# Performance work log

Hardware: AMD Instinct MI355X
Metric: run time of the kernel (lower is better)

The kernel has to match this reference:

```python
import jax, jax.numpy as jnp
from jax import lax
import numpy as np

NPOINTS = 1024
B, N, C = 32, 100000, 3


def setup_inputs() -> dict:
    key = jax.random.key(0)
    k1, k2 = jax.random.split(key)
    coord = jax.random.normal(k1, (B, N, C), dtype=jnp.float32)
    farthest_init = jax.random.randint(k2, (B,), 0, N, dtype=jnp.int64)
    return {"coord": coord, "farthest_init": farthest_init}


def reference(coord, farthest_init):
    # coord: (B, N, 3); farthest_init: (B,) seed indices.
    Bs, Ns, _ = coord.shape
    init_distance = jnp.full((Bs, Ns), 1e10, dtype=coord.dtype)

    def step(carry, _):
        distance, farthest = carry
        # gather current centroid per batch: (B, 1, 3)
        centroid = jnp.take_along_axis(coord, farthest[:, None, None], axis=1)
        dist = jnp.sum((coord - centroid) ** 2, axis=-1)  # (B, N)
        distance = jnp.minimum(distance, dist)            # masked update
        new_farthest = jnp.argmax(distance, axis=-1)      # (B,)
        # record the index that was just used as centroid (pre-update), as in torch loop
        return (distance, new_farthest), farthest

    (_, _), centroids_t = lax.scan(step, (init_distance, farthest_init), None, length=NPOINTS)
    centroids = centroids_t.T  # (B, NPOINTS)
    # gather sampled coordinates: (B, NPOINTS, 3)
    sampled = jnp.take_along_axis(coord, centroids[:, :, None], axis=1)
    return centroids, sampled
```

## Files before the change

### kernel.cpp

```cpp
#include <hip/hip_runtime.h>
#include <stdint.h>

#define BATCHES 32
#define NPT     100000
#define NSAMP   1024
#define GPB     16
#define NPAIR   16
#define TPB     1024
#define NCW     15
#define CTH     (NCW*64)
#define PPB     6250
#define PPT     7
#define TAILT   490

typedef unsigned long long u64;
typedef unsigned int u32;

#define WS_BYTES (2 * BATCHES * GPB * 4 * 8)

__device__ __forceinline__ void red_ki(u64& key, u32& idx, int off) {
    u64 ok = __shfl_xor(key, off, 64);
    u32 oi = __shfl_xor(idx, off, 64);
    if (ok > key || (ok == key && oi < idx)) { key = ok; idx = oi; }
}

__device__ __forceinline__ void red_step(u64& key, u32& idx, float& x, float& y, float& z, int off) {
    u64   ok = __shfl_xor(key, off, 64);
    u32   oi = __shfl_xor(idx, off, 64);
    float ox = __shfl_xor(x, off, 64);
    float oy = __shfl_xor(y, off, 64);
    float oz = __shfl_xor(z, off, 64);
    if (ok > key || (ok == key && oi < idx)) { key = ok; idx = oi; x = ox; y = oy; z = oz; }
}

__global__ void
__attribute__((amdgpu_flat_work_group_size(TPB, TPB), amdgpu_waves_per_eu(4, 4)))
fps_kernel(const float* __restrict__ coord,
           const int* __restrict__ seed_raw,
           float* __restrict__ out,
           u64* __restrict__ rec)
{
    const int tid  = threadIdx.x;
    const int lane = tid & 63;
    const int wid  = tid >> 6;
    const int p    = (int)blockIdx.x & (NPAIR - 1);
    const int g    = (int)blockIdx.x >> 4;
    const int base = g * PPB;
    const int bA = p, bB = p + NPAIR;

    __shared__ u64 winw[2][2][2];
    __shared__ u32 sbar[8];
    __shared__ u64   pkey[2][NCW];
    __shared__ u32   pidx[2][NCW];
    __shared__ float pxs[2][NCW], pys[2][NCW], pzs[2][NCW];

    if (tid < 8) { sbar[tid] = 0; ((u64*)winw)[tid] = 0ull; }
    __syncthreads();

    float* cent_out = out;
    float* samp_out = out + BATCHES * NSAMP;

    if (wid == NCW) {
        for (int t = 1; t < NSAMP; ++t) {
            #pragma unroll
            for (int xb = 0; xb < 2; ++xb) {
                const int batch = xb ? bB : bA;
                u64* slot = rec + ((size_t)((t & 1) * BATCHES + batch) * GPB) * 4;
                const u64 t2 = (u64)(((t >> 1) + 1) & 3);
                const bool mine = lane < 3 * GPB;
                u64* wp = slot + (mine ? ((lane / 3) * 4 + (lane % 3)) : 0);
                u64 w = 0;
                for (;;) {
                    bool ok = true;
                    if (mine) {
                        w = __hip_atomic_load(wp, __ATOMIC_RELAXED, __HIP_MEMORY_SCOPE_AGENT);
                        ok = (w >> 62) == t2;
                    }
                    if (__ballot(ok) == ~0ull) break;
                    __builtin_amdgcn_s_sleep(1);
                }
                const int li = lane & 15;
                u64 w0 = __shfl(w, 3 * li + 0, 64);
                u64 w1 = __shfl(w, 3 * li + 1, 64);
                u64 w2 = __shfl(w, 3 * li + 2, 64);
                u64 k3 = 0ull; u32 i3 = 0xFFFFFFFFu; float x3 = 0.f, y3 = 0.f, z3 = 0.f;
                if (lane < GPB) {
                    k3 = (w0 & 0x3FFFFFFFFFFFFFFFull) | (((w1 >> 60) & 3ull) << 62);
                    u32 xbt = (u32)(w1 >> 28);
                    u32 ybt = (u32)(((w1 & 0xFFFFFFFull) << 4) | ((w2 >> 58) & 0xFull));
                    u32 zbt = (u32)(w2 >> 26);
                    i3 = (u32)((w2 >> 9) & 0x1FFFFu);
                    x3 = __uint_as_float(xbt); y3 = __uint_as_float(ybt); z3 = __uint_as_float(zbt);
                }
                red_step(k3, i3, x3, y3, z3, 8); red_step(k3, i3, x3, y3, z3, 4);
                red_step(k3, i3, x3, y3, z3, 2); red_step(k3, i3, x3, y3, z3, 1);
                if (lane == 0) {
                    u32 xbt = __float_as_uint(x3), ybt = __float_as_uint(y3), zbt = __float_as_uint(z3);
                    u64 v0 = (t2 << 62) | ((u64)xbt << 30) | (u64)(ybt >> 2);
                    u64 v1 = (t2 << 62) | ((u64)(ybt & 3u) << 60) | ((u64)zbt << 28) | ((u64)i3 << 11);
                    __hip_atomic_store(&winw[xb][t & 1][0], v0, __ATOMIC_RELAXED, __HIP_MEMORY_SCOPE_WORKGROUP);
                    __hip_atomic_store(&winw[xb][t & 1][1], v1, __ATOMIC_RELAXED, __HIP_MEMORY_SCOPE_WORKGROUP);
                }
            }
        }
        return;
    }

    const int ct = tid;
    const float* cbA = coord + (size_t)bA * (NPT * 3);
    const float* cbB = coord + (size_t)bB * (NPT * 3);

    int odd = 0;
    #pragma unroll
    for (int i = 1; i < 32; i += 2) odd |= seed_raw[i];
    u32 scur[2]; float scx[2], scy[2], scz[2];
    scur[0] = (u32)((odd == 0) ? seed_raw[2 * bA] : seed_raw[bA]);
    scur[1] = (u32)((odd == 0) ? seed_raw[2 * bB] : seed_raw[bB]);
    scx[0] = cbA[(size_t)scur[0] * 3 + 0]; scy[0] = cbA[(size_t)scur[0] * 3 + 1]; scz[0] = cbA[(size_t)scur[0] * 3 + 2];
    scx[1] = cbB[(size_t)scur[1] * 3 + 0]; scy[1] = cbB[(size_t)scur[1] * 3 + 1]; scz[1] = cbB[(size_t)scur[1] * 3 + 2];

    float  px[2][PPT], py[2][PPT], pz[2][PPT];
    double d[2][PPT];
    #pragma unroll
    for (int xb = 0; xb < 2; ++xb) {
        const float* cb = xb ? cbB : cbA;
        #pragma unroll
        for (int k = 0; k < PPT; ++k) {
            bool v = (k < PPT - 1) || (ct < TAILT);
            int gi = base + (v ? (k * CTH + ct) : 0);
            px[xb][k] = v ? cb[(size_t)gi * 3 + 0] : 0.f;
            py[xb][k] = v ? cb[(size_t)gi * 3 + 1] : 0.f;
            pz[xb][k] = v ? cb[(size_t)gi * 3 + 2] : 0.f;
            d[xb][k]  = v ? 1.0e10 : 0.0;
        }
    }

    for (int t = 0; t < NSAMP; ++t) {
        #pragma unroll
        for (int xb = 0; xb < 2; ++xb) {
            const int batch = xb ? bB : bA;
            const int pi = 2 * t + xb;
            u32 cur; float cx, cy, cz;
            if (t == 0) {
                cur = scur[xb]; cx = scx[xb]; cy = scy[xb]; cz = scz[xb];
            } else {
                const u64 t2 = (u64)(((t >> 1) + 1) & 3);
                u64 v0, v1;
                for (;;) {
                    v0 = __hip_atomic_load(&winw[xb][t & 1][0], __ATOMIC_RELAXED, __HIP_MEMORY_SCOPE_WORKGROUP);
                    v1 = __hip_atomic_load(&winw[xb][t & 1][1], __ATOMIC_RELAXED, __HIP_MEMORY_SCOPE_WORKGROUP);
                    if (((v0 >> 62) == t2) & ((v1 >> 62) == t2)) break;
                }
                u32 xbt = (u32)(v0 >> 30);
                u32 ybt = (u32)(((v0 & 0x3FFFFFFFull) << 2) | ((v1 >> 60) & 3ull));
                u32 zbt = (u32)(v1 >> 28);
                cur = (u32)((v1 >> 11) & 0x1FFFFu);
                cx = __uint_as_float(xbt); cy = __uint_as_float(ybt); cz = __uint_as_float(zbt);
            }
            if (g == 0 && wid == 1 && lane == 0) {
                cent_out[batch * NSAMP + t] = (float)cur;
                size_t so = ((size_t)batch * NSAMP + t) * 3;
                samp_out[so + 0] = cx; samp_out[so + 1] = cy; samp_out[so + 2] = cz;
            }
            if (t == NSAMP - 1) continue;

            const double cxd = (double)cx, cyd = (double)cy, czd = (double)cz;
            double bd = -1.0; u32 bi = 0; float bx = 0.f, by = 0.f, bz = 0.f;
            #pragma unroll
            for (int k = 0; k < PPT; ++k) {
                if (k == PPT - 1 && ct >= TAILT) break;
                double dx = __dsub_rn((double)px[xb][k], cxd);
                double dy = __dsub_rn((double)py[xb][k], cyd);
                double dz = __dsub_rn((double)pz[xb][k], czd);
                double d2 = __dadd_rn(__dadd_rn(__dmul_rn(dx, dx), __dmul_rn(dy, dy)),
                                      __dmul_rn(dz, dz));
                double nd = fmin(d[xb][k], d2);
                d[xb][k] = nd;
                bool gt = nd > bd;
                bd = gt ? nd : bd;
                bi = gt ? (u32)(base + k * CTH + ct) : bi;
                bx = gt ? px[xb][k] : bx;
                by = gt ? py[xb][k] : by;
                bz = gt ? pz[xb][k] : bz;
            }
            u64 key = (u64)__double_as_longlong(bd);

            u64 wk = key; u32 wi = bi;
            red_ki(wk, wi, 32); red_ki(wk, wi, 16); red_ki(wk, wi, 8);
            red_ki(wk, wi, 4);  red_ki(wk, wi, 2);  red_ki(wk, wi, 1);
            const int pb = pi & 1;
            if (wi == bi) { pkey[pb][wid] = wk; pidx[pb][wid] = wi;
                            pxs[pb][wid] = bx; pys[pb][wid] = by; pzs[pb][wid] = bz; }

            if (lane == 0)
                __hip_atomic_fetch_add(&sbar[pi & 7], 1u, __ATOMIC_RELEASE, __HIP_MEMORY_SCOPE_WORKGROUP);
            const u32 tgt = (u32)(NCW * ((pi >> 3) + 1));
            while (__hip_atomic_load(&sbar[pi & 7], __ATOMIC_ACQUIRE, __HIP_MEMORY_SCOPE_WORKGROUP) < tgt) {}

            if (wid == 0) {
                u64   k2 = (lane < NCW) ? pkey[pb][lane] : 0ull;
                u32   i2 = (lane < NCW) ? pidx[pb][lane] : 0xFFFFFFFFu;
                float x2 = (lane < NCW) ? pxs[pb][lane] : 0.f;
                float y2 = (lane < NCW) ? pys[pb][lane] : 0.f;
                float z2 = (lane < NCW) ? pzs[pb][lane] : 0.f;
                red_step(k2, i2, x2, y2, z2, 8); red_step(k2, i2, x2, y2, z2, 4);
                red_step(k2, i2, x2, y2, z2, 2); red_step(k2, i2, x2, y2, z2, 1);
                if (lane == 0) {
                    const u32 v = (u32)(t + 1);
                    const u64 t2p = (u64)(((v >> 1) + 1) & 3);
                    u64* r = rec + ((size_t)((v & 1) * BATCHES + batch) * GPB + g) * 4;
                    u32 xbt = __float_as_uint(x2), ybt = __float_as_uint(y2), zbt = __float_as_uint(z2);
                    u64 w0 = (t2p << 62) | (k2 & 0x3FFFFFFFFFFFFFFFull);
                    u64 w1 = (t2p << 62) | ((k2 >> 62) << 60) | ((u64)xbt << 28) | (u64)(ybt >> 4);
                    u64 w2 = (t2p << 62) | ((u64)(ybt & 0xFu) << 58) | ((u64)zbt << 26) | ((u64)i2 << 9);
                    __hip_atomic_store(&r[0], w0, __ATOMIC_RELAXED, __HIP_MEMORY_SCOPE_AGENT);
                    __hip_atomic_store(&r[1], w1, __ATOMIC_RELAXED, __HIP_MEMORY_SCOPE_AGENT);
                    __hip_atomic_store(&r[2], w2, __ATOMIC_RELAXED, __HIP_MEMORY_SCOPE_AGENT);
                }
            }
        }
    }
}

extern "C" void kernel_launch(void* const* d_in, const int* in_sizes, int n_in,
                              void* d_out, int out_size, void* d_ws, size_t ws_size,
                              hipStream_t stream)
{
    const float* coord = (const float*)d_in[0];
    const int*   seed  = (const int*)d_in[1];
    float* out = (float*)d_out;
    u64* rec = (u64*)d_ws;

    hipMemsetAsync(d_ws, 0, WS_BYTES, stream);
    fps_kernel<<<dim3(NPAIR * GPB), dim3(TPB), 0, stream>>>(coord, seed, out, rec);
}
```

Before: 4.390 ms.

## Poll both batches' records together, defer coordinate selection, and narrow barrier wait

The coordinator wave now polls both paired batches' global records in one combined loop, with each lane loading two words. It reduces each batch as soon as that batch's records are ready, instead of waiting on them one after the other. The compute loop no longer carries best-point coordinates through every iteration; only the winning lane recovers them afterwards with a select. The intra-block spin wait is moved so that only wave 0 waits on the counter, letting the other compute waves go ahead to the next step. This cuts polling latency and per-iteration register work, but other waves now rely on the double-buffered shared slots and the later handoff for ordering.

Measured after the change: 7.751 ms. 1.77x slower.

```diff
diff --git a/kernel.cpp b/kernel.cpp
--- a/kernel.cpp
+++ b/kernel.cpp
@@ -62,45 +62,52 @@
 
     if (wid == NCW) {
         for (int t = 1; t < NSAMP; ++t) {
-            #pragma unroll
-            for (int xb = 0; xb < 2; ++xb) {
-                const int batch = xb ? bB : bA;
-                u64* slot = rec + ((size_t)((t & 1) * BATCHES + batch) * GPB) * 4;
-                const u64 t2 = (u64)(((t >> 1) + 1) & 3);
-                const bool mine = lane < 3 * GPB;
-                u64* wp = slot + (mine ? ((lane / 3) * 4 + (lane % 3)) : 0);
-                u64 w = 0;
-                for (;;) {
-                    bool ok = true;
-                    if (mine) {
-                        w = __hip_atomic_load(wp, __ATOMIC_RELAXED, __HIP_MEMORY_SCOPE_AGENT);
-                        ok = (w >> 62) == t2;
+            const u64 t2 = (u64)(((t >> 1) + 1) & 3);
+            const size_t regA = ((size_t)((t & 1) * BATCHES + bA) * GPB) * 4;
+            const size_t regB = ((size_t)((t & 1) * BATCHES + bB) * GPB) * 4;
+            u64* ad = rec + ((lane < 32) ? (regA + 2 * lane) : (regB + 2 * (lane - 32)));
+            bool dA = false, dB = false;
+            u64 wlo = 0, whi = 0;
+            for (;;) {
+                wlo = __hip_atomic_load(&ad[0], __ATOMIC_RELAXED, __HIP_MEMORY_SCOPE_AGENT);
+                whi = __hip_atomic_load(&ad[1], __ATOMIC_RELAXED, __HIP_MEMORY_SCOPE_AGENT);
+                bool ok0 = (wlo >> 62) == t2;
+                bool ok1 = (whi >> 62) == t2;
+                bool ok  = ((lane & 1) == 0) ? (ok0 && ok1) : ok0;
+                u64 bal = __ballot(ok);
+                #pragma unroll
+                for (int xb = 0; xb < 2; ++xb) {
+                    bool done = xb ? dB : dA;
+                    u64 msk = xb ? 0xFFFFFFFF00000000ull : 0x00000000FFFFFFFFull;
+                    if (!done && (bal & msk) == msk) {
+                        const int srcBase = xb ? 32 : 0;
+                        int sj = srcBase + 2 * (lane & 15);
+                        u64 w0 = __shfl(wlo, sj, 64);
+                        u64 w1 = __shfl(whi, sj, 64);
+                        u64 w2 = __shfl(wlo, sj + 1, 64);
+                        u64 k3 = 0ull; u32 i3 = 0xFFFFFFFFu; float x3 = 0.f, y3 = 0.f, z3 = 0.f;
+                        if (lane < GPB) {
+                            k3 = (w0 & 0x3FFFFFFFFFFFFFFFull) | (((w1 >> 60) & 3ull) << 62);
+                            u32 xbt = (u32)(w1 >> 28);
+                            u32 ybt = (u32)(((w1 & 0xFFFFFFFull) << 4) | ((w2 >> 58) & 0xFull));
+                            u32 zbt = (u32)(w2 >> 26);
+                            i3 = (u32)((w2 >> 9) & 0x1FFFFu);
+                            x3 = __uint_as_float(xbt); y3 = __uint_as_float(ybt); z3 = __uint_as_float(zbt);
+                        }
+                        red_step(k3, i3, x3, y3, z3, 8); red_step(k3, i3, x3, y3, z3, 4);
+                        red_step(k3, i3, x3, y3, z3, 2); red_step(k3, i3, x3, y3, z3, 1);
+                        if (lane == 0) {
+                            u32 xbt = __float_as_uint(x3), ybt = __float_as_uint(y3), zbt = __float_as_uint(z3);
+                            u64 v0 = (t2 << 62) | ((u64)xbt << 30) | (u64)(ybt >> 2);
+                            u64 v1 = (t2 << 62) | ((u64)(ybt & 3u) << 60) | ((u64)zbt << 28) | ((u64)i3 << 11);
+                            __hip_atomic_store(&winw[xb][t & 1][0], v0, __ATOMIC_RELAXED, __HIP_MEMORY_SCOPE_WORKGROUP);
+                            __hip_atomic_store(&winw[xb][t & 1][1], v1, __ATOMIC_RELAXED, __HIP_MEMORY_SCOPE_WORKGROUP);
+                        }
+                        if (xb) dB = true; else dA = true;
                     }
-                    if (__ballot(ok) == ~0ull) break;
-                    __builtin_amdgcn_s_sleep(1);
-                }
-                const int li = lane & 15;
-                u64 w0 = __shfl(w, 3 * li + 0, 64);
-                u64 w1 = __shfl(w, 3 * li + 1, 64);
-                u64 w2 = __shfl(w, 3 * li + 2, 64);
-                u64 k3 = 0ull; u32 i3 = 0xFFFFFFFFu; float x3 = 0.f, y3 = 0.f, z3 = 0.f;
-                if (lane < GPB) {
-                    k3 = (w0 & 0x3FFFFFFFFFFFFFFFull) | (((w1 >> 60) & 3ull) << 62);
-                    u32 xbt = (u32)(w1 >> 28);
-                    u32 ybt = (u32)(((w1 & 0xFFFFFFFull) << 4) | ((w2 >> 58) & 0xFull));
-                    u32 zbt = (u32)(w2 >> 26);
-                    i3 = (u32)((w2 >> 9) & 0x1FFFFu);
-                    x3 = __uint_as_float(xbt); y3 = __uint_as_float(ybt); z3 = __uint_as_float(zbt);
-                }
-                red_step(k3, i3, x3, y3, z3, 8); red_step(k3, i3, x3, y3, z3, 4);
-                red_step(k3, i3, x3, y3, z3, 2); red_step(k3, i3, x3, y3, z3, 1);
-                if (lane == 0) {
-                    u32 xbt = __float_as_uint(x3), ybt = __float_as_uint(y3), zbt = __float_as_uint(z3);
-                    u64 v0 = (t2 << 62) | ((u64)xbt << 30) | (u64)(ybt >> 2);
-                    u64 v1 = (t2 << 62) | ((u64)(ybt & 3u) << 60) | ((u64)zbt << 28) | ((u64)i3 << 11);
-                    __hip_atomic_store(&winw[xb][t & 1][0], v0, __ATOMIC_RELAXED, __HIP_MEMORY_SCOPE_WORKGROUP);
-                    __hip_atomic_store(&winw[xb][t & 1][1], v1, __ATOMIC_RELAXED, __HIP_MEMORY_SCOPE_WORKGROUP);
-                }
+                }
+                if (dA && dB) break;
+                __builtin_amdgcn_s_sleep(1);
             }
         }
         return;
@@ -165,7 +172,7 @@
             if (t == NSAMP - 1) continue;
 
             const double cxd = (double)cx, cyd = (double)cy, czd = (double)cz;
-            double bd = -1.0; u32 bi = 0; float bx = 0.f, by = 0.f, bz = 0.f;
+            double bd = -1.0; u32 bi = 0;
             #pragma unroll
             for (int k = 0; k < PPT; ++k) {
                 if (k == PPT - 1 && ct >= TAILT) break;
@@ -179,9 +186,6 @@
                 bool gt = nd > bd;
                 bd = gt ? nd : bd;
                 bi = gt ? (u32)(base + k * CTH + ct) : bi;
-                bx = gt ? px[xb][k] : bx;
-                by = gt ? py[xb][k] : by;
-                bz = gt ? pz[xb][k] : bz;
             }
             u64 key = (u64)__double_as_longlong(bd);
 
@@ -189,15 +193,25 @@
             red_ki(wk, wi, 32); red_ki(wk, wi, 16); red_ki(wk, wi, 8);
             red_ki(wk, wi, 4);  red_ki(wk, wi, 2);  red_ki(wk, wi, 1);
             const int pb = pi & 1;
-            if (wi == bi) { pkey[pb][wid] = wk; pidx[pb][wid] = wi;
-                            pxs[pb][wid] = bx; pys[pb][wid] = by; pzs[pb][wid] = bz; }
+            if (wi == bi) {
+                float bx = px[xb][0], by = py[xb][0], bz = pz[xb][0];
+                #pragma unroll
+                for (int k = 1; k < PPT; ++k) {
+                    bool m = (bi == (u32)(base + k * CTH + ct));
+                    bx = m ? px[xb][k] : bx;
+                    by = m ? py[xb][k] : by;
+                    bz = m ? pz[xb][k] : bz;
+                }
+                pkey[pb][wid] = wk; pidx[pb][wid] = wi;
+                pxs[pb][wid] = bx; pys[pb][wid] = by; pzs[pb][wid] = bz;
+            }
 
             if (lane == 0)
                 __hip_atomic_fetch_add(&sbar[pi & 7], 1u, __ATOMIC_RELEASE, __HIP_MEMORY_SCOPE_WORKGROUP);
-            const u32 tgt = (u32)(NCW * ((pi >> 3) + 1));
-            while (__hip_atomic_load(&sbar[pi & 7], __ATOMIC_ACQUIRE, __HIP_MEMORY_SCOPE_WORKGROUP) < tgt) {}
 
             if (wid == 0) {
+                const u32 tgt = (u32)(NCW * ((pi >> 3) + 1));
+                while (__hip_atomic_load(&sbar[pi & 7], __ATOMIC_ACQUIRE, __HIP_MEMORY_SCOPE_WORKGROUP) < tgt) {}
                 u64   k2 = (lane < NCW) ? pkey[pb][lane] : 0ull;
                 u32   i2 = (lane < NCW) ? pidx[pb][lane] : 0xFFFFFFFFu;
                 float x2 = (lane < NCW) ? pxs[pb][lane] : 0.f;
```

## Split block-level reduce/publish into dedicated wave, decoupling compute waves from barrier

Applied to the files above, without the earlier changes.

Cuts the compute waves from 15 to 14 and adds a dedicated wave that waits on the shared-memory counter barrier, reduces the per-wave winners and publishes the packed record to global memory. Compute waves no longer spin on the barrier after each half-step, so the critical path no longer includes wave 0's reduction and store. The per-point argmax loop now tracks only distance and index, and the winning lane recovers its coordinates afterwards, which frees registers in the hot loop. The cost is fewer waves sharing the distance work, with a larger tail, plus tighter coupling through the lockstep shared-memory slots.

Result: slower. 6.943 ms (+58.2%).

```diff
diff --git a/kernel.cpp b/kernel.cpp
--- a/kernel.cpp
+++ b/kernel.cpp
@@ -7,11 +7,11 @@
 #define GPB     16
 #define NPAIR   16
 #define TPB     1024
-#define NCW     15
+#define NCW     14
 #define CTH     (NCW*64)
 #define PPB     6250
 #define PPT     7
-#define TAILT   490
+#define TAILT   874
 
 typedef unsigned long long u64;
 typedef unsigned int u32;
@@ -48,8 +48,8 @@
     const int base = g * PPB;
     const int bA = p, bB = p + NPAIR;
 
-    __shared__ u64 winw[2][2][2];
-    __shared__ u32 sbar[8];
+    __shared__ u64   winw[2][2][2];
+    __shared__ u32   sbar[8];
     __shared__ u64   pkey[2][NCW];
     __shared__ u32   pidx[2][NCW];
     __shared__ float pxs[2][NCW], pys[2][NCW], pzs[2][NCW];
@@ -61,12 +61,42 @@
     float* samp_out = out + BATCHES * NSAMP;
 
     if (wid == NCW) {
-        for (int t = 1; t < NSAMP; ++t) {
+        for (int t = 0; t < NSAMP - 1; ++t) {
             #pragma unroll
             for (int xb = 0; xb < 2; ++xb) {
-                const int batch = xb ? bB : bA;
-                u64* slot = rec + ((size_t)((t & 1) * BATCHES + batch) * GPB) * 4;
-                const u64 t2 = (u64)(((t >> 1) + 1) & 3);
+                const int pi = 2 * t + xb;
+                const u32 tgt = (u32)(NCW * ((pi >> 3) + 1));
+                while (__hip_atomic_load(&sbar[pi & 7], __ATOMIC_ACQUIRE, __HIP_MEMORY_SCOPE_WORKGROUP) < tgt) {}
+                u64   k2 = (lane < NCW) ? pkey[pi & 1][lane] : 0ull;
+                u32   i2 = (lane < NCW) ? pidx[pi & 1][lane] : 0xFFFFFFFFu;
+                float x2 = (lane < NCW) ? pxs[pi & 1][lane] : 0.f;
+                float y2 = (lane < NCW) ? pys[pi & 1][lane] : 0.f;
+                float z2 = (lane < NCW) ? pzs[pi & 1][lane] : 0.f;
+                red_step(k2, i2, x2, y2, z2, 8); red_step(k2, i2, x2, y2, z2, 4);
+                red_step(k2, i2, x2, y2, z2, 2); red_step(k2, i2, x2, y2, z2, 1);
+                if (lane == 0) {
+                    const u32 v = (u32)(t + 1);
+                    const u64 t2p = (u64)(((v >> 1) + 1) & 3);
+                    u64* r = rec + ((size_t)((v & 1) * BATCHES + (xb ? bB : bA)) * GPB + g) * 4;
+                    u32 xbt = __float_as_uint(x2), ybt = __float_as_uint(y2), zbt = __float_as_uint(z2);
+                    u64 w0 = (t2p << 62) | (k2 & 0x3FFFFFFFFFFFFFFFull);
+                    u64 w1 = (t2p << 62) | ((k2 >> 62) << 60) | ((u64)xbt << 28) | (u64)(ybt >> 4);
+                    u64 w2 = (t2p << 62) | ((u64)(ybt & 0xFu) << 58) | ((u64)zbt << 26) | ((u64)i2 << 9);
+                    __hip_atomic_store(&r[0], w0, __ATOMIC_RELAXED, __HIP_MEMORY_SCOPE_AGENT);
+                    __hip_atomic_store(&r[1], w1, __ATOMIC_RELAXED, __HIP_MEMORY_SCOPE_AGENT);
+                    __hip_atomic_store(&r[2], w2, __ATOMIC_RELAXED, __HIP_MEMORY_SCOPE_AGENT);
+                }
+            }
+        }
+        return;
+    }
+
+    if (wid == NCW + 1) {
+        for (int t = 1; t < NSAMP; ++t) {
+            const u64 t2 = (u64)(((t >> 1) + 1) & 3);
+            #pragma unroll
+            for (int xb = 0; xb < 2; ++xb) {
+                u64* slot = rec + ((size_t)((t & 1) * BATCHES + (xb ? bB : bA)) * GPB) * 4;
                 const bool mine = lane < 3 * GPB;
                 u64* wp = slot + (mine ? ((lane / 3) * 4 + (lane % 3)) : 0);
                 u64 w = 0;
@@ -165,7 +195,7 @@
             if (t == NSAMP - 1) continue;
 
             const double cxd = (double)cx, cyd = (double)cy, czd = (double)cz;
-            double bd = -1.0; u32 bi = 0; float bx = 0.f, by = 0.f, bz = 0.f;
+            double bd = -1.0; u32 bi = 0;
             #pragma unroll
             for (int k = 0; k < PPT; ++k) {
                 if (k == PPT - 1 && ct >= TAILT) break;
@@ -179,45 +209,26 @@
                 bool gt = nd > bd;
                 bd = gt ? nd : bd;
                 bi = gt ? (u32)(base + k * CTH + ct) : bi;
-                bx = gt ? px[xb][k] : bx;
-                by = gt ? py[xb][k] : by;
-                bz = gt ? pz[xb][k] : bz;
             }
             u64 key = (u64)__double_as_longlong(bd);
 
             u64 wk = key; u32 wi = bi;
             red_ki(wk, wi, 32); red_ki(wk, wi, 16); red_ki(wk, wi, 8);
             red_ki(wk, wi, 4);  red_ki(wk, wi, 2);  red_ki(wk, wi, 1);
-            const int pb = pi & 1;
-            if (wi == bi) { pkey[pb][wid] = wk; pidx[pb][wid] = wi;
-                            pxs[pb][wid] = bx; pys[pb][wid] = by; pzs[pb][wid] = bz; }
-
+            if (wi == bi) {
+                float bx = px[xb][0], by = py[xb][0], bz = pz[xb][0];
+                #pragma unroll
+                for (int k = 1; k < PPT; ++k) {
+                    bool m = (bi == (u32)(base + k * CTH + ct));
+                    bx = m ? px[xb][k] : bx;
+                    by = m ? py[xb][k] : by;
+                    bz = m ? pz[xb][k] : bz;
+                }
+                pkey[pi & 1][wid] = wk; pidx[pi & 1][wid] = wi;
+                pxs[pi & 1][wid] = bx; pys[pi & 1][wid] = by; pzs[pi & 1][wid] = bz;
+            }
             if (lane == 0)
                 __hip_atomic_fetch_add(&sbar[pi & 7], 1u, __ATOMIC_RELEASE, __HIP_MEMORY_SCOPE_WORKGROUP);
-            const u32 tgt = (u32)(NCW * ((pi >> 3) + 1));
-            while (__hip_atomic_load(&sbar[pi & 7], __ATOMIC_ACQUIRE, __HIP_MEMORY_SCOPE_WORKGROUP) < tgt) {}
-
-            if (wid == 0) {
-                u64   k2 = (lane < NCW) ? pkey[pb][lane] : 0ull;
-                u32   i2 = (lane < NCW) ? pidx[pb][lane] : 0xFFFFFFFFu;
-                float x2 = (lane < NCW) ? pxs[pb][lane] : 0.f;
-                float y2 = (lane < NCW) ? pys[pb][lane] : 0.f;
-                float z2 = (lane < NCW) ? pzs[pb][lane] : 0.f;
-                red_step(k2, i2, x2, y2, z2, 8); red_step(k2, i2, x2, y2, z2, 4);
-                red_step(k2, i2, x2, y2, z2, 2); red_step(k2, i2, x2, y2, z2, 1);
-                if (lane == 0) {
-                    const u32 v = (u32)(t + 1);
-                    const u64 t2p = (u64)(((v >> 1) + 1) & 3);
-                    u64* r = rec + ((size_t)((v & 1) * BATCHES + batch) * GPB + g) * 4;
-                    u32 xbt = __float_as_uint(x2), ybt = __float_as_uint(y2), zbt = __float_as_uint(z2);
-                    u64 w0 = (t2p << 62) | (k2 & 0x3FFFFFFFFFFFFFFFull);
-                    u64 w1 = (t2p << 62) | ((k2 >> 62) << 60) | ((u64)xbt << 28) | (u64)(ybt >> 4);
-                    u64 w2 = (t2p << 62) | ((u64)(ybt & 0xFu) << 58) | ((u64)zbt << 26) | ((u64)i2 << 9);
-                    __hip_atomic_store(&r[0], w0, __ATOMIC_RELAXED, __HIP_MEMORY_SCOPE_AGENT);
-                    __hip_atomic_store(&r[1], w1, __ATOMIC_RELAXED, __HIP_MEMORY_SCOPE_AGENT);
-                    __hip_atomic_store(&r[2], w2, __ATOMIC_RELAXED, __HIP_MEMORY_SCOPE_AGENT);
-                }
-            }
         }
     }
 }
```
